# Optimization experiments

Hardware: AMD Instinct MI355X
Metric: run time of the kernel (lower is better)

The kernel has to match this reference:

```python
import jax, jax.numpy as jnp
import numpy as np
import math

DIM = 96; HEADS = 3; WS = 4; SS = 2; RES = 48; B = 2
N = WS ** 3  # tokens per window
LOG2_8 = math.log2(8.0)


def _rel_coords_table():
    c = np.arange(-(WS - 1), WS, dtype=np.float32)
    t = np.stack(np.meshgrid(c, c, c, indexing='ij'), axis=-1)
    t = t / (WS - 1)
    t = t * 8.0
    t = np.sign(t) * np.log2(np.abs(t) + 1.0) / LOG2_8
    return t.reshape(-1, 3)


def _rel_pos_index():
    coords = np.stack(np.meshgrid(np.arange(WS), np.arange(WS), np.arange(WS), indexing='ij'))
    cf = coords.reshape(3, -1)
    rel = (cf[:, :, None] - cf[:, None, :]).transpose(1, 2, 0).copy()
    rel[:, :, 0] += WS - 1; rel[:, :, 1] += WS - 1; rel[:, :, 2] += WS - 1
    rel[:, :, 0] *= (2 * WS - 1) * (2 * WS - 1)
    rel[:, :, 1] *= (2 * WS - 1)
    return rel.sum(-1).reshape(-1)  # (N*N,)


def _attn_mask():
    H = W = D = RES
    img = np.zeros((H, W, D), np.float32)
    cnt = 0
    sl = (slice(0, -WS), slice(-WS, -SS), slice(-SS, None))
    for h in sl:
        for w in sl:
            for d in sl:
                img[h, w, d] = cnt
                cnt += 1
    m = img.reshape(H // WS, WS, W // WS, WS, D // WS, WS)
    m = m.transpose(0, 2, 4, 1, 3, 5).reshape(-1, N)
    am = m[:, None, :] - m[:, :, None]
    return np.where(am != 0, np.float32(-100.0), np.float32(0.0))  # (nW, N, N)


def _win_part(x):
    Bx, H, W, D, C = x.shape
    x = x.reshape(Bx, H // WS, WS, W // WS, WS, D // WS, WS, C)
    x = x.transpose(0, 1, 3, 5, 2, 4, 6, 7)
    return x.reshape(-1, N, C)


def _win_rev(w, Bx, H, W, D):
    C = w.shape[-1]
    x = w.reshape(Bx, H // WS, W // WS, D // WS, WS, WS, WS, C)
    x = x.transpose(0, 1, 4, 2, 5, 3, 6, 7)
    return x.reshape(Bx, H, W, D, C)


def _ln(x, g, b, eps=1e-5):
    mu = jnp.mean(x, axis=-1, keepdims=True)
    var = jnp.mean(jnp.square(x - mu), axis=-1, keepdims=True)
    return (x - mu) * jax.lax.rsqrt(var + eps) * g + b


def setup_inputs() -> dict:
    key = jax.random.key(0)
    ks = jax.random.split(key, 8)
    s = 0.02
    return {
        'x': jax.random.normal(ks[0], (B, RES, RES, RES, DIM), jnp.float32),
        'qkv_w': jax.random.normal(ks[1], (3 * DIM, DIM), jnp.float32) * s,
        'q_bias': jnp.zeros((DIM,), jnp.float32),
        'v_bias': jnp.zeros((DIM,), jnp.float32),
        'logit_scale': jnp.full((HEADS, 1, 1), math.log(10.0), jnp.float32),
        'cpb_w1': jax.random.normal(ks[2], (512, 3), jnp.float32) * s,
        'cpb_b1': jnp.zeros((512,), jnp.float32),
        'cpb_w2': jax.random.normal(ks[3], (HEADS, 512), jnp.float32) * s,
        'proj_w': jax.random.normal(ks[4], (DIM, DIM), jnp.float32) * s,
        'proj_b': jnp.zeros((DIM,), jnp.float32),
        'norm1_g': jnp.ones((DIM,), jnp.float32),
        'norm1_b': jnp.zeros((DIM,), jnp.float32),
        'fc1_w': jax.random.normal(ks[5], (4 * DIM, DIM), jnp.float32) * s,
        'fc1_b': jnp.zeros((4 * DIM,), jnp.float32),
        'fc2_w': jax.random.normal(ks[6], (DIM, 4 * DIM), jnp.float32) * s,
        'fc2_b': jnp.zeros((DIM,), jnp.float32),
        'norm2_g': jnp.ones((DIM,), jnp.float32),
        'norm2_b': jnp.zeros((DIM,), jnp.float32),
    }


def reference(x, qkv_w, q_bias, v_bias, logit_scale, cpb_w1, cpb_b1, cpb_w2,
              proj_w, proj_b, norm1_g, norm1_b, fc1_w, fc1_b, fc2_w, fc2_b,
              norm2_g, norm2_b):
    Bx, H, W, D, C = x.shape
    hd = C // HEADS
    rct = jnp.asarray(_rel_coords_table())
    rpi = _rel_pos_index()
    amask = jnp.asarray(_attn_mask())  # (nW, N, N)

    # cyclic shift + window partition
    shifted = jnp.roll(x, (-SS, -SS, -SS), axis=(1, 2, 3))
    xw = _win_part(shifted)  # (B*nW, N, C)
    B_ = xw.shape[0]; nW = B_ // Bx

    # qkv (k has no bias in SwinV2)
    bias = jnp.concatenate([q_bias, jnp.zeros_like(q_bias), v_bias])
    qkv = (xw @ qkv_w.T + bias).reshape(B_, N, 3, HEADS, hd).transpose(2, 0, 3, 1, 4)
    q, k, v = qkv[0], qkv[1], qkv[2]

    # cosine attention with clamped learnable logit scale
    qn = q / jnp.maximum(jnp.linalg.norm(q, axis=-1, keepdims=True), 1e-12)
    kn = k / jnp.maximum(jnp.linalg.norm(k, axis=-1, keepdims=True), 1e-12)
    attn = jnp.einsum('bhnd,bhmd->bhnm', qn, kn)
    scale = jnp.exp(jnp.minimum(logit_scale, math.log(1.0 / 0.01)))  # (HEADS,1,1)
    attn = attn * scale[None]

    # continuous relative position bias via small MLP + lookup
    tbl = jax.nn.relu(rct @ cpb_w1.T + cpb_b1) @ cpb_w2.T  # (T, HEADS)
    rpb = tbl[rpi].reshape(N, N, HEADS).transpose(2, 0, 1)
    rpb = 16.0 * jax.nn.sigmoid(rpb)
    attn = attn + rpb[None]

    # shift-window mask + softmax
    attn = attn.reshape(Bx, nW, HEADS, N, N) + amask[None, :, None]
    attn = jax.nn.softmax(attn.reshape(B_, HEADS, N, N), axis=-1)

    out = jnp.einsum('bhnm,bhmd->bnhd', attn, v).reshape(B_, N, C)
    out = out @ proj_w.T + proj_b

    # reverse windows + reverse shift
    aw = _win_rev(out.reshape(B_, WS, WS, WS, C), Bx, H, W, D)
    aw = jnp.roll(aw, (SS, SS, SS), axis=(1, 2, 3))

    # SwinV2 post-norm residuals
    x = x + _ln(aw, norm1_g, norm1_b)
    h = jax.nn.gelu(x @ fc1_w.T + fc1_b, approximate=False) @ fc2_w.T + fc2_b
    x = x + _ln(h, norm2_g, norm2_b)
    return x
```

## Files before the change

kernel.cpp:

```cpp
#include <hip/hip_runtime.h>
#include <math.h>

#define RES   48
#define WS    4
#define SSH   2
#define DIM   96
#define HEADS 3
#define HD    32
#define NTOK  64
#define NWAX  12
#define NWIN  (NWAX*NWAX*NWAX)

#define TSTR 104
#define VSTR 72
#define PSTR 72
#define H_STR 392

typedef float f32x4 __attribute__((ext_vector_type(4)));
typedef short s16x8 __attribute__((ext_vector_type(8)));

__device__ __forceinline__ short f2bf(float f) {
    unsigned u = __builtin_bit_cast(unsigned, f);
    u = (u + 0x7FFFu + ((u >> 16) & 1u)) >> 16;
    return (short)u;
}
__device__ __forceinline__ float bf2f(short s) {
    unsigned u = ((unsigned)(unsigned short)s) << 16;
    return __builtin_bit_cast(float, u);
}
__device__ __forceinline__ float gelu_f(float a) {
    float z = a*(1.5957691216057308f + 0.07135481627159927f*a*a);
    return a / (1.0f + __expf(-z));
}
__device__ __forceinline__ int region(int g) {
    return (g < RES - WS) ? 0 : ((g < RES - SSH) ? 1 : 2);
}

__global__ void prep_kernel(const float* __restrict__ cw1, const float* __restrict__ cb1,
                            const float* __restrict__ cw2,
                            const float* __restrict__ fc1_w, const float* __restrict__ fc2_w,
                            const float* __restrict__ qkv_w, const float* __restrict__ proj_w,
                            float* __restrict__ tbl,
                            short* __restrict__ w1p, short* __restrict__ w2p,
                            short* __restrict__ qkvp, short* __restrict__ projp) {
    int bid = blockIdx.x;
    if (bid < 343) {
        __shared__ float hid[512];
        int ti = bid;
        int a = ti / 49, b = (ti / 7) % 7, c = ti % 7;
        float comp[3] = {(float)(a - 3), (float)(b - 3), (float)(c - 3)};
        float f[3];
        #pragma unroll
        for (int k = 0; k < 3; ++k) {
            float u = (comp[k] / 3.0f) * 8.0f;
            float s = (u > 0.f) ? 1.f : ((u < 0.f) ? -1.f : 0.f);
            f[k] = s * log2f(fabsf(u) + 1.0f) * (1.0f / 3.0f);
        }
        for (int j = threadIdx.x; j < 512; j += blockDim.x) {
            float acc = cb1[j] + f[0]*cw1[j*3+0] + f[1]*cw1[j*3+1] + f[2]*cw1[j*3+2];
            hid[j] = fmaxf(acc, 0.f);
        }
        __syncthreads();
        int tid = threadIdx.x;
        if (tid < 192) {
            int h = tid >> 6, lane = tid & 63;
            float p = 0.f;
            for (int j = lane; j < 512; j += 64) p += cw2[h*512 + j] * hid[j];
            #pragma unroll
            for (int off = 32; off; off >>= 1) p += __shfl_down(p, off, 64);
            if (lane == 0) tbl[ti*3 + h] = p;
        }
    } else if (bid < 343 + 144) {
        int i = (bid - 343)*256 + threadIdx.x;
        if (i >= 36864) return;
        {
            int o = i / 96, c = i - o*96;
            int tile = (o >> 4)*3 + (c >> 5);
            int lane = ((c >> 3) & 3)*16 + (o & 15);
            w1p[tile*512 + lane*8 + (c & 7)] = f2bf(fc1_w[i]);
        }
        {
            int co = i / 384, oo = i - co*384;
            int tile = (co >> 4)*12 + (oo >> 5);
            int lane = ((oo >> 3) & 3)*16 + (co & 15);
            w2p[tile*512 + lane*8 + (oo & 7)] = f2bf(fc2_w[i]);
        }
    } else {
        int i = (bid - 487)*256 + threadIdx.x;
        if (i < 288*96) {
            int o = i / 96, c = i - o*96;
            int tile = (o >> 4)*3 + (c >> 5);
            int lane = ((c >> 3) & 3)*16 + (o & 15);
            qkvp[tile*512 + lane*8 + (c & 7)] = f2bf(qkv_w[i]);
        }
        if (i < 96*96) {
            int co = i / 96, k = i - co*96;
            int tile = (co >> 4)*3 + (k >> 5);
            int lane = ((k >> 3) & 3)*16 + (co & 15);
            projp[tile*512 + lane*8 + (k & 7)] = f2bf(proj_w[i]);
        }
    }
}

__global__ void rpb_kernel(const float* __restrict__ tbl, float* __restrict__ rpb) {
    int bi = blockIdx.x;
    int h = bi >> 6, i = bi & 63;
    int j = threadIdx.x;
    int hi = i >> 4, wi = (i >> 2) & 3, di = i & 3;
    int hj = j >> 4, wj = (j >> 2) & 3, dj = j & 3;
    int idx = (hi - hj + 3)*49 + (wi - wj + 3)*7 + (di - dj + 3);
    float v = tbl[idx*3 + h];
    rpb[(h*64 + i)*64 + j] = 16.0f / (1.0f + expf(-v));
}

__global__ __launch_bounds__(256, 2)
void swin_fused_kernel(const float* __restrict__ x, const short* __restrict__ qkvp,
                       const float* __restrict__ q_bias, const float* __restrict__ v_bias,
                       const float* __restrict__ logit_scale,
                       const short* __restrict__ projp, const float* __restrict__ proj_b,
                       const float* __restrict__ rpb,
                       const float* __restrict__ g1, const float* __restrict__ b1v,
                       const short* __restrict__ w1p, const float* __restrict__ fc1_b,
                       const short* __restrict__ w2p, const float* __restrict__ fc2_b,
                       const float* __restrict__ g2, const float* __restrict__ b2v,
                       float* __restrict__ out) {
    __shared__ __align__(16) char pool[64768];
    int*   xbase = (int*)(pool + 0);
    int*   cnt_s = (int*)(pool + 256);
    float* knorm = (float*)(pool + 512);
    short* x_s   = (short*)(pool + 1280);
    short* q_s   = (short*)(pool + 14592);
    short* k_s   = (short*)(pool + 27904);
    short* vT    = (short*)(pool + 41216);
    short* p_s   = (short*)(pool + 55040);
    short* x1b   = x_s;
    short* hb    = (short*)(pool + 14592);
    short* ao_s  = q_s;

    int tid = threadIdx.x;
    int l   = tid & 63;
    int w   = __builtin_amdgcn_readfirstlane(tid >> 6);
    int lc  = l & 15;
    int lg  = l >> 4;

    int wid = blockIdx.x;
    int b   = wid / NWIN;
    int rem = wid - b*NWIN;
    int wh = rem / (NWAX*NWAX);
    int ww = (rem / NWAX) % NWAX;
    int wd = rem % NWAX;

    if (tid < NTOK) {
        int t = tid;
        int lh = t >> 4, lw = (t >> 2) & 3, ld = t & 3;
        int gh = wh*WS + lh, gw = ww*WS + lw, gd = wd*WS + ld;
        int sh = (gh + SSH) % RES, sw = (gw + SSH) % RES, sd = (gd + SSH) % RES;
        xbase[t] = (((b*RES + sh)*RES + sw)*RES + sd)*DIM;
        cnt_s[t] = region(gh)*9 + region(gw)*3 + region(gd);
    }
    __syncthreads();

    for (int idx = tid; idx < NTOK*12; idx += 256) {
        int r = idx / 12, g = idx - r*12;
        const float* src = x + xbase[r] + g*8;
        float4 a = *reinterpret_cast<const float4*>(src);
        float4 c = *reinterpret_cast<const float4*>(src + 4);
        s16x8 v;
        v[0]=f2bf(a.x); v[1]=f2bf(a.y); v[2]=f2bf(a.z); v[3]=f2bf(a.w);
        v[4]=f2bf(c.x); v[5]=f2bf(c.y); v[6]=f2bf(c.z); v[7]=f2bf(c.w);
        *reinterpret_cast<s16x8*>(&x_s[r*TSTR + g*8]) = v;
    }
    __syncthreads();

    {
        s16x8 af[3][4];
        #pragma unroll
        for (int ks = 0; ks < 3; ++ks)
            #pragma unroll
            for (int m = 0; m < 4; ++m)
                af[ks][m] = *reinterpret_cast<const s16x8*>(&x_s[(m*16+lc)*TSTR + ks*32 + lg*8]);

        for (int nt = w; nt < 18; nt += 4) {
            int col = nt*16 + lc;
            float bias = 0.f;
            if (nt < 6) bias = q_bias[col];
            else if (nt >= 12) bias = v_bias[col - 192];
            f32x4 C[4];
            #pragma unroll
            for (int m = 0; m < 4; ++m) C[m] = f32x4{bias, bias, bias, bias};
            #pragma unroll
            for (int ks = 0; ks < 3; ++ks) {
                s16x8 bf = *reinterpret_cast<const s16x8*>(&qkvp[(nt*3+ks)*512 + l*8]);
                #pragma unroll
                for (int m = 0; m < 4; ++m)
                    C[m] = __builtin_amdgcn_mfma_f32_16x16x32_bf16(af[ks][m], bf, C[m], 0, 0, 0);
            }
            if (nt < 6) {
                #pragma unroll
                for (int m = 0; m < 4; ++m)
                    #pragma unroll
                    for (int r = 0; r < 4; ++r)
                        q_s[(m*16+lg*4+r)*TSTR + col] = f2bf(C[m][r]);
            } else if (nt < 12) {
                #pragma unroll
                for (int m = 0; m < 4; ++m)
                    #pragma unroll
                    for (int r = 0; r < 4; ++r)
                        k_s[(m*16+lg*4+r)*TSTR + col - 96] = f2bf(C[m][r]);
            } else {
                #pragma unroll
                for (int m = 0; m < 4; ++m)
                    #pragma unroll
                    for (int r = 0; r < 4; ++r)
                        vT[(col-192)*VSTR + m*16+lg*4+r] = f2bf(C[m][r]);
            }
        }
    }
    __syncthreads();

    if (tid < 192) {
        int h = tid >> 6, i = tid & 63;
        float n = 0.f;
        #pragma unroll
        for (int c = 0; c < 4; ++c) {
            s16x8 v = *reinterpret_cast<const s16x8*>(&k_s[i*TSTR + h*32 + c*8]);
            #pragma unroll
            for (int e = 0; e < 8; ++e) { float f = bf2f(v[e]); n += f*f; }
        }
        knorm[h*64 + i] = 1.0f / fmaxf(sqrtf(n), 1e-12f);

        s16x8 qv[4];
        float qn = 0.f;
        #pragma unroll
        for (int c = 0; c < 4; ++c) {
            qv[c] = *reinterpret_cast<const s16x8*>(&q_s[i*TSTR + h*32 + c*8]);
            #pragma unroll
            for (int e = 0; e < 8; ++e) { float f = bf2f(qv[c][e]); qn += f*f; }
        }
        float sc = __expf(fminf(logit_scale[h], 4.605170185988092f));
        float qr = sc / fmaxf(sqrtf(qn), 1e-12f);
        #pragma unroll
        for (int c = 0; c < 4; ++c) {
            s16x8 o;
            #pragma unroll
            for (int e = 0; e < 8; ++e) o[e] = f2bf(bf2f(qv[c][e]) * qr);
            *reinterpret_cast<s16x8*>(&q_s[i*TSTR + h*32 + c*8]) = o;
        }
    }
    __syncthreads();

    f32x4 sc_[3][4];
    {
        s16x8 aq[3];
        #pragma unroll
        for (int h = 0; h < 3; ++h)
            aq[h] = *reinterpret_cast<const s16x8*>(&q_s[(w*16+lc)*TSTR + h*32 + lg*8]);
        #pragma unroll
        for (int h = 0; h < 3; ++h)
            #pragma unroll
            for (int nt = 0; nt < 4; ++nt) {
                s16x8 bk = *reinterpret_cast<const s16x8*>(&k_s[(nt*16+lc)*TSTR + h*32 + lg*8]);
                sc_[h][nt] = __builtin_amdgcn_mfma_f32_16x16x32_bf16(aq[h], bk, f32x4{0.f,0.f,0.f,0.f}, 0, 0, 0);
            }
    }

    int ci[4];
    #pragma unroll
    for (int r = 0; r < 4; ++r) ci[r] = cnt_s[w*16 + lg*4 + r];
    int cjv[4];
    #pragma unroll
    for (int nt = 0; nt < 4; ++nt) cjv[nt] = cnt_s[nt*16 + lc];

    #pragma unroll
    for (int h = 0; h < 3; ++h) {
        #pragma unroll
        for (int nt = 0; nt < 4; ++nt) {
            float kn = knorm[h*64 + nt*16 + lc];
            int cj = cjv[nt];
            #pragma unroll
            for (int r = 0; r < 4; ++r) {
                int row = w*16 + lg*4 + r;
                float s = sc_[h][nt][r]*kn + rpb[(h*64 + row)*64 + nt*16 + lc];
                if (ci[r] != cj) s -= 100.0f;
                sc_[h][nt][r] = s;
            }
        }
        float linv[4];
        #pragma unroll
        for (int r = 0; r < 4; ++r) {
            float mm = fmaxf(fmaxf(sc_[h][0][r], sc_[h][1][r]), fmaxf(sc_[h][2][r], sc_[h][3][r]));
            #pragma unroll
            for (int msk = 1; msk < 16; msk <<= 1) mm = fmaxf(mm, __shfl_xor(mm, msk, 64));
            float ll = 0.f;
            #pragma unroll
            for (int nt = 0; nt < 4; ++nt) {
                float ee = __expf(sc_[h][nt][r] - mm);
                sc_[h][nt][r] = ee;
                ll += ee;
            }
            #pragma unroll
            for (int msk = 1; msk < 16; msk <<= 1) ll += __shfl_xor(ll, msk, 64);
            linv[r] = 1.0f / ll;
        }
        #pragma unroll
        for (int nt = 0; nt < 4; ++nt)
            #pragma unroll
            for (int r = 0; r < 4; ++r)
                p_s[(w*16+lg*4+r)*PSTR + nt*16 + lc] = f2bf(sc_[h][nt][r]);

        f32x4 o0 = {0.f,0.f,0.f,0.f}, o1 = {0.f,0.f,0.f,0.f};
        #pragma unroll
        for (int ks = 0; ks < 2; ++ks) {
            s16x8 ap = *reinterpret_cast<const s16x8*>(&p_s[(w*16+lc)*PSTR + ks*32 + lg*8]);
            s16x8 b0 = *reinterpret_cast<const s16x8*>(&vT[(h*32 + lc)*VSTR + ks*32 + lg*8]);
            s16x8 b1 = *reinterpret_cast<const s16x8*>(&vT[(h*32 + 16 + lc)*VSTR + ks*32 + lg*8]);
            o0 = __builtin_amdgcn_mfma_f32_16x16x32_bf16(ap, b0, o0, 0, 0, 0);
            o1 = __builtin_amdgcn_mfma_f32_16x16x32_bf16(ap, b1, o1, 0, 0, 0);
        }
        #pragma unroll
        for (int r = 0; r < 4; ++r) {
            ao_s[(w*16+lg*4+r)*TSTR + h*32 + lc]      = f2bf(o0[r]*linv[r]);
            ao_s[(w*16+lg*4+r)*TSTR + h*32 + 16 + lc] = f2bf(o1[r]*linv[r]);
        }
    }

    float yv[6][4];
    {
        s16x8 aa[3];
        #pragma unroll
        for (int ks = 0; ks < 3; ++ks)
            aa[ks] = *reinterpret_cast<const s16x8*>(&ao_s[(w*16+lc)*TSTR + ks*32 + lg*8]);
        #pragma unroll
        for (int nt = 0; nt < 6; ++nt) {
            float bias = proj_b[nt*16 + lc];
            f32x4 C = f32x4{bias, bias, bias, bias};
            #pragma unroll
            for (int ks = 0; ks < 3; ++ks) {
                s16x8 bf = *reinterpret_cast<const s16x8*>(&projp[(nt*3+ks)*512 + l*8]);
                C = __builtin_amdgcn_mfma_f32_16x16x32_bf16(aa[ks], bf, C, 0, 0, 0);
            }
            #pragma unroll
            for (int r = 0; r < 4; ++r) yv[nt][r] = C[r];
        }
    }
    __syncthreads();

    float x1v[6][4];
    #pragma unroll
    for (int r = 0; r < 4; ++r) {
        float s = 0.f, sq = 0.f;
        #pragma unroll
        for (int n = 0; n < 6; ++n) { float v = yv[n][r]; s += v; sq += v*v; }
        #pragma unroll
        for (int m = 1; m < 16; m <<= 1) { s += __shfl_xor(s, m, 64); sq += __shfl_xor(sq, m, 64); }
        float mu  = s * (1.0f/DIM);
        float var = sq * (1.0f/DIM) - mu*mu;
        float rs  = rsqrtf(fmaxf(var, 0.f) + 1e-5f);
        int t = w*16 + lg*4 + r;
        #pragma unroll
        for (int n = 0; n < 6; ++n) {
            int c = n*16 + lc;
            float xf = bf2f(x_s[t*TSTR + c]);
            float v = xf + (yv[n][r] - mu)*rs*g1[c] + b1v[c];
            x1v[n][r] = v;
            x1b[t*TSTR + c] = f2bf(v);
        }
    }
    __syncthreads();

    {
        f32x4 acc1[4][6];
        #pragma unroll
        for (int n = 0; n < 6; ++n) {
            float bb = fc1_b[w*96 + n*16 + lc];
            #pragma unroll
            for (int m = 0; m < 4; ++m) acc1[m][n] = f32x4{bb, bb, bb, bb};
        }
        #pragma unroll
        for (int ks = 0; ks < 3; ++ks) {
            s16x8 af[4];
            #pragma unroll
            for (int m = 0; m < 4; ++m)
                af[m] = *reinterpret_cast<const s16x8*>(&x1b[(m*16 + lc)*TSTR + ks*32 + lg*8]);
            #pragma unroll
            for (int n = 0; n < 6; ++n) {
                s16x8 bf = *reinterpret_cast<const s16x8*>(&w1p[((w*6 + n)*3 + ks)*512 + l*8]);
                #pragma unroll
                for (int m = 0; m < 4; ++m)
                    acc1[m][n] = __builtin_amdgcn_mfma_f32_16x16x32_bf16(af[m], bf, acc1[m][n], 0, 0, 0);
            }
        }
        #pragma unroll
        for (int m = 0; m < 4; ++m) {
            #pragma unroll
            for (int n = 0; n < 6; ++n) {
                int col = w*96 + n*16 + lc;
                #pragma unroll
                for (int r = 0; r < 4; ++r) {
                    int row = m*16 + lg*4 + r;
                    hb[row*H_STR + col] = f2bf(gelu_f(acc1[m][n][r]));
                }
            }
        }
    }
    __syncthreads();

    {
        f32x4 acc2[6];
        #pragma unroll
        for (int n = 0; n < 6; ++n) {
            float bb = fc2_b[n*16 + lc];
            acc2[n] = f32x4{bb, bb, bb, bb};
        }
        #pragma unroll
        for (int ks = 0; ks < 12; ++ks) {
            s16x8 af = *reinterpret_cast<const s16x8*>(&hb[(w*16 + lc)*H_STR + ks*32 + lg*8]);
            #pragma unroll
            for (int n = 0; n < 6; ++n) {
                s16x8 bf = *reinterpret_cast<const s16x8*>(&w2p[(n*12 + ks)*512 + l*8]);
                acc2[n] = __builtin_amdgcn_mfma_f32_16x16x32_bf16(af, bf, acc2[n], 0, 0, 0);
            }
        }
        #pragma unroll
        for (int r = 0; r < 4; ++r) {
            float s = 0.f, sq = 0.f;
            #pragma unroll
            for (int n = 0; n < 6; ++n) { float v = acc2[n][r]; s += v; sq += v*v; }
            #pragma unroll
            for (int m = 1; m < 16; m <<= 1) { s += __shfl_xor(s, m, 64); sq += __shfl_xor(sq, m, 64); }
            float mu  = s * (1.0f/DIM);
            float var = sq * (1.0f/DIM) - mu*mu;
            float rs  = rsqrtf(fmaxf(var, 0.f) + 1e-5f);
            int t = w*16 + lg*4 + r;
            int xb = xbase[t];
            #pragma unroll
            for (int n = 0; n < 6; ++n) {
                int c = n*16 + lc;
                out[xb + c] = x1v[n][r] + (acc2[n][r] - mu)*rs*g2[c] + b2v[c];
            }
        }
    }
}

extern "C" void kernel_launch(void* const* d_in, const int* in_sizes, int n_in,
                              void* d_out, int out_size, void* d_ws, size_t ws_size,
                              hipStream_t stream) {
    const float* x      = (const float*)d_in[0];
    const float* qkv_w  = (const float*)d_in[1];
    const float* q_bias = (const float*)d_in[2];
    const float* v_bias = (const float*)d_in[3];
    const float* lscale = (const float*)d_in[4];
    const float* cpb_w1 = (const float*)d_in[5];
    const float* cpb_b1 = (const float*)d_in[6];
    const float* cpb_w2 = (const float*)d_in[7];
    const float* proj_w = (const float*)d_in[8];
    const float* proj_b = (const float*)d_in[9];
    const float* n1g    = (const float*)d_in[10];
    const float* n1b    = (const float*)d_in[11];
    const float* fc1_w  = (const float*)d_in[12];
    const float* fc1_b  = (const float*)d_in[13];
    const float* fc2_w  = (const float*)d_in[14];
    const float* fc2_b  = (const float*)d_in[15];
    const float* n2g    = (const float*)d_in[16];
    const float* n2b    = (const float*)d_in[17];
    float* out = (float*)d_out;

    char* wsb = (char*)d_ws;
    float* tbl  = (float*)wsb;
    float* rpb  = (float*)(wsb + 8192);
    short* w1p  = (short*)(wsb + 65536);
    short* w2p  = (short*)(wsb + 65536 + 73728);
    short* qkvp = (short*)(wsb + 65536 + 147456);
    short* projp= qkvp + 27648;

    prep_kernel<<<595, 256, 0, stream>>>(cpb_w1, cpb_b1, cpb_w2, fc1_w, fc2_w,
                                         qkv_w, proj_w, tbl, w1p, w2p, qkvp, projp);
    rpb_kernel<<<192, 64, 0, stream>>>(tbl, rpb);
    swin_fused_kernel<<<2*NWIN, 256, 0, stream>>>(x, qkvp, q_bias, v_bias, lscale,
                                                  projp, proj_b, rpb,
                                                  n1g, n1b, w1p, fc1_b, w2p, fc2_b,
                                                  n2g, n2b, out);
}
```

Measured before the change: 194.0 us.

## Split MLP hidden into two halves to shrink LDS and raise occupancy

```diff
diff --git a/kernel.cpp b/kernel.cpp
--- a/kernel.cpp
+++ b/kernel.cpp
@@ -14,7 +14,7 @@
 #define TSTR 104
 #define VSTR 72
 #define PSTR 72
-#define H_STR 392
+#define HSTR 200
 
 typedef float f32x4 __attribute__((ext_vector_type(4)));
 typedef short s16x8 __attribute__((ext_vector_type(8)));
@@ -27,6 +27,11 @@
 __device__ __forceinline__ float bf2f(short s) {
     unsigned u = ((unsigned)(unsigned short)s) << 16;
     return __builtin_bit_cast(float, u);
+}
+__device__ __forceinline__ unsigned cvt_pk(float lo, float hi) {
+    unsigned r;
+    asm("v_cvt_pk_bf16_f32 %0, %1, %2" : "=v"(r) : "v"(lo), "v"(hi));
+    return r;
 }
 __device__ __forceinline__ float gelu_f(float a) {
     float z = a*(1.5957691216057308f + 0.07135481627159927f*a*a);
@@ -75,7 +80,9 @@
         if (i >= 36864) return;
         {
             int o = i / 96, c = i - o*96;
-            int tile = (o >> 4)*3 + (c >> 5);
+            int H = o / 192, rem = o - H*192;
+            int wv = rem / 48, n3 = (rem - wv*48) >> 4;
+            int tile = ((H*12 + wv*3 + n3)*3) + (c >> 5);
             int lane = ((c >> 3) & 3)*16 + (o & 15);
             w1p[tile*512 + lane*8 + (c & 7)] = f2bf(fc1_w[i]);
         }
@@ -113,7 +120,7 @@
     rpb[(h*64 + i)*64 + j] = 16.0f / (1.0f + expf(-v));
 }
 
-__global__ __launch_bounds__(256, 2)
+__global__ __launch_bounds__(256, 3)
 void swin_fused_kernel(const float* __restrict__ x, const short* __restrict__ qkvp,
                        const float* __restrict__ q_bias, const float* __restrict__ v_bias,
                        const float* __restrict__ logit_scale,
@@ -124,18 +131,17 @@
                        const short* __restrict__ w2p, const float* __restrict__ fc2_b,
                        const float* __restrict__ g2, const float* __restrict__ b2v,
                        float* __restrict__ out) {
-    __shared__ __align__(16) char pool[64768];
+    __shared__ __align__(16) char pool[54272];
     int*   xbase = (int*)(pool + 0);
     int*   cnt_s = (int*)(pool + 256);
-    float* knorm = (float*)(pool + 512);
-    short* x_s   = (short*)(pool + 1280);
-    short* q_s   = (short*)(pool + 14592);
-    short* k_s   = (short*)(pool + 27904);
-    short* vT    = (short*)(pool + 41216);
-    short* p_s   = (short*)(pool + 55040);
+    short* x_s   = (short*)(pool + 512);
+    short* q_s   = (short*)(pool + 13824);
+    short* k_s   = (short*)(pool + 27136);
+    short* vT    = (short*)(pool + 40448);
+    short* p_s   = k_s;
+    short* ao_s  = q_s;
     short* x1b   = x_s;
-    short* hb    = (short*)(pool + 14592);
-    short* ao_s  = q_s;
+    short* hb    = (short*)(pool + 13824);
 
     int tid = threadIdx.x;
     int l   = tid & 63;
@@ -160,15 +166,32 @@
     }
     __syncthreads();
 
+    int ci[4], cjv[4];
+    #pragma unroll
+    for (int r = 0; r < 4; ++r) ci[r] = cnt_s[w*16 + lg*4 + r];
+    #pragma unroll
+    for (int nt = 0; nt < 4; ++nt) cjv[nt] = cnt_s[nt*16 + lc];
+    float biasv[3][4][4];
+    #pragma unroll
+    for (int h = 0; h < 3; ++h)
+        #pragma unroll
+        for (int nt = 0; nt < 4; ++nt)
+            #pragma unroll
+            for (int r = 0; r < 4; ++r) {
+                int row = w*16 + lg*4 + r;
+                float bv = rpb[(h*64 + row)*64 + nt*16 + lc];
+                biasv[h][nt][r] = (ci[r] != cjv[nt]) ? bv - 100.0f : bv;
+            }
+
     for (int idx = tid; idx < NTOK*12; idx += 256) {
         int r = idx / 12, g = idx - r*12;
         const float* src = x + xbase[r] + g*8;
         float4 a = *reinterpret_cast<const float4*>(src);
         float4 c = *reinterpret_cast<const float4*>(src + 4);
-        s16x8 v;
-        v[0]=f2bf(a.x); v[1]=f2bf(a.y); v[2]=f2bf(a.z); v[3]=f2bf(a.w);
-        v[4]=f2bf(c.x); v[5]=f2bf(c.y); v[6]=f2bf(c.z); v[7]=f2bf(c.w);
-        *reinterpret_cast<s16x8*>(&x_s[r*TSTR + g*8]) = v;
+        uint4 v;
+        v.x = cvt_pk(a.x, a.y); v.y = cvt_pk(a.z, a.w);
+        v.z = cvt_pk(c.x, c.y); v.w = cvt_pk(c.z, c.w);
+        *reinterpret_cast<uint4*>(&x_s[r*TSTR + g*8]) = v;
     }
     __syncthreads();
 
@@ -197,54 +220,81 @@
             }
             if (nt < 6) {
                 #pragma unroll
-                for (int m = 0; m < 4; ++m)
-                    #pragma unroll
-                    for (int r = 0; r < 4; ++r)
-                        q_s[(m*16+lg*4+r)*TSTR + col] = f2bf(C[m][r]);
+                for (int m = 0; m < 4; ++m) {
+                    unsigned pA = cvt_pk(C[m][0], C[m][1]);
+                    unsigned pB = cvt_pk(C[m][2], C[m][3]);
+                    int row = m*16 + lg*4;
+                    q_s[(row+0)*TSTR + col] = (short)pA;
+                    q_s[(row+1)*TSTR + col] = (short)(pA >> 16);
+                    q_s[(row+2)*TSTR + col] = (short)pB;
+                    q_s[(row+3)*TSTR + col] = (short)(pB >> 16);
+                }
             } else if (nt < 12) {
                 #pragma unroll
-                for (int m = 0; m < 4; ++m)
-                    #pragma unroll
-                    for (int r = 0; r < 4; ++r)
-                        k_s[(m*16+lg*4+r)*TSTR + col - 96] = f2bf(C[m][r]);
+                for (int m = 0; m < 4; ++m) {
+                    unsigned pA = cvt_pk(C[m][0], C[m][1]);
+                    unsigned pB = cvt_pk(C[m][2], C[m][3]);
+                    int row = m*16 + lg*4;
+                    k_s[(row+0)*TSTR + col - 96] = (short)pA;
+                    k_s[(row+1)*TSTR + col - 96] = (short)(pA >> 16);
+                    k_s[(row+2)*TSTR + col - 96] = (short)pB;
+                    k_s[(row+3)*TSTR + col - 96] = (short)(pB >> 16);
+                }
             } else {
                 #pragma unroll
-                for (int m = 0; m < 4; ++m)
-                    #pragma unroll
-                    for (int r = 0; r < 4; ++r)
-                        vT[(col-192)*VSTR + m*16+lg*4+r] = f2bf(C[m][r]);
-            }
-        }
-    }
-    __syncthreads();
-
-    if (tid < 192) {
-        int h = tid >> 6, i = tid & 63;
-        float n = 0.f;
-        #pragma unroll
-        for (int c = 0; c < 4; ++c) {
-            s16x8 v = *reinterpret_cast<const s16x8*>(&k_s[i*TSTR + h*32 + c*8]);
-            #pragma unroll
-            for (int e = 0; e < 8; ++e) { float f = bf2f(v[e]); n += f*f; }
-        }
-        knorm[h*64 + i] = 1.0f / fmaxf(sqrtf(n), 1e-12f);
-
-        s16x8 qv[4];
-        float qn = 0.f;
-        #pragma unroll
-        for (int c = 0; c < 4; ++c) {
-            qv[c] = *reinterpret_cast<const s16x8*>(&q_s[i*TSTR + h*32 + c*8]);
-            #pragma unroll
-            for (int e = 0; e < 8; ++e) { float f = bf2f(qv[c][e]); qn += f*f; }
-        }
-        float sc = __expf(fminf(logit_scale[h], 4.605170185988092f));
-        float qr = sc / fmaxf(sqrtf(qn), 1e-12f);
-        #pragma unroll
-        for (int c = 0; c < 4; ++c) {
-            s16x8 o;
-            #pragma unroll
-            for (int e = 0; e < 8; ++e) o[e] = f2bf(bf2f(qv[c][e]) * qr);
-            *reinterpret_cast<s16x8*>(&q_s[i*TSTR + h*32 + c*8]) = o;
+                for (int m = 0; m < 4; ++m) {
+                    uint2 pv;
+                    pv.x = cvt_pk(C[m][0], C[m][1]);
+                    pv.y = cvt_pk(C[m][2], C[m][3]);
+                    *reinterpret_cast<uint2*>(&vT[(col-192)*VSTR + m*16 + lg*4]) = pv;
+                }
+            }
+        }
+    }
+    __syncthreads();
+
+    if (w < 3) {
+        int h = w, i = l;
+        {
+            s16x8 kv[4];
+            float kn = 0.f;
+            #pragma unroll
+            for (int c = 0; c < 4; ++c) {
+                kv[c] = *reinterpret_cast<const s16x8*>(&k_s[i*TSTR + h*32 + c*8]);
+                #pragma unroll
+                for (int e = 0; e < 8; ++e) { float f = bf2f(kv[c][e]); kn += f*f; }
+            }
+            float kr = 1.0f / fmaxf(sqrtf(kn), 1e-12f);
+            #pragma unroll
+            for (int c = 0; c < 4; ++c) {
+                uint4 o;
+                o.x = cvt_pk(bf2f(kv[c][0])*kr, bf2f(kv[c][1])*kr);
+                o.y = cvt_pk(bf2f(kv[c][2])*kr, bf2f(kv[c][3])*kr);
+                o.z = cvt_pk(bf2f(kv[c][4])*kr, bf2f(kv[c][5])*kr);
+                o.w = cvt_pk(bf2f(kv[c][6])*kr, bf2f(kv[c][7])*kr);
+                *reinterpret_cast<uint4*>(&k_s[i*TSTR + h*32 + c*8]) = o;
+            }
+        }
+        {
+            s16x8 qv[4];
+            float qn = 0.f;
+            #pragma unroll
+            for (int c = 0; c < 4; ++c) {
+                qv[c] = *reinterpret_cast<const s16x8*>(&q_s[i*TSTR + h*32 + c*8]);
+                #pragma unroll
+                for (int e = 0; e < 8; ++e) { float f = bf2f(qv[c][e]); qn += f*f; }
+            }
+            float sc = __expf(fminf(logit_scale[h], 4.605170185988092f));
+            float qr = sc / fmaxf(sqrtf(qn), 1e-12f);
+            #pragma unroll
+            for (int c = 0; c < 4; ++c) {
+                uint4 o;
+                o.x = cvt_pk(bf2f(qv[c][0])*qr, bf2f(qv[c][1])*qr);
+                o.y = cvt_pk(bf2f(qv[c][2])*qr, bf2f(qv[c][3])*qr);
+                o.z = cvt_pk(bf2f(qv[c][4])*qr, bf2f(qv[c][5])*qr);
+                o.w = cvt_pk(bf2f(qv[c][6])*qr, bf2f(qv[c][7])*qr);
+                *reinterpret_cast<uint4*>(&q_s[i*TSTR + h*32 + c*8]) = o;
+            }
         }
     }
     __syncthreads();
@@ -263,28 +313,15 @@
                 sc_[h][nt] = __builtin_amdgcn_mfma_f32_16x16x32_bf16(aq[h], bk, f32x4{0.f,0.f,0.f,0.f}, 0, 0, 0);
             }
     }
-
-    int ci[4];
-    #pragma unroll
-    for (int r = 0; r < 4; ++r) ci[r] = cnt_s[w*16 + lg*4 + r];
-    int cjv[4];
-    #pragma unroll
-    for (int nt = 0; nt < 4; ++nt) cjv[nt] = cnt_s[nt*16 + lc];
+    __syncthreads();
 
     #pragma unroll
     for (int h = 0; h < 3; ++h) {
         #pragma unroll
-        for (int nt = 0; nt < 4; ++nt) {
-            float kn = knorm[h*64 + nt*16 + lc];
-            int cj = cjv[nt];
-            #pragma unroll
-            for (int r = 0; r < 4; ++r) {
-                int row = w*16 + lg*4 + r;
-                float s = sc_[h][nt][r]*kn + rpb[(h*64 + row)*64 + nt*16 + lc];
-                if (ci[r] != cj) s -= 100.0f;
-                sc_[h][nt][r] = s;
-            }
-        }
+        for (int nt = 0; nt < 4; ++nt)
+            #pragma unroll
+            for (int r = 0; r < 4; ++r)
+                sc_[h][nt][r] += biasv[h][nt][r];
         float linv[4];
         #pragma unroll
         for (int r = 0; r < 4; ++r) {
@@ -303,10 +340,15 @@
             linv[r] = 1.0f / ll;
         }
         #pragma unroll
-        for (int nt = 0; nt < 4; ++nt)
-            #pragma unroll
-            for (int r = 0; r < 4; ++r)
-                p_s[(w*16+lg*4+r)*PSTR + nt*16 + lc] = f2bf(sc_[h][nt][r]);
+        for (int nt = 0; nt < 4; ++nt) {
+            unsigned pA = cvt_pk(sc_[h][nt][0], sc_[h][nt][1]);
+            unsigned pB = cvt_pk(sc_[h][nt][2], sc_[h][nt][3]);
+            int row = w*16 + lg*4;
+            p_s[(row+0)*PSTR + nt*16 + lc] = (short)pA;
+            p_s[(row+1)*PSTR + nt*16 + lc] = (short)(pA >> 16);
+            p_s[(row+2)*PSTR + nt*16 + lc] = (short)pB;
+            p_s[(row+3)*PSTR + nt*16 + lc] = (short)(pB >> 16);
+        }
 
         f32x4 o0 = {0.f,0.f,0.f,0.f}, o1 = {0.f,0.f,0.f,0.f};
         #pragma unroll
@@ -317,10 +359,20 @@
             o0 = __builtin_amdgcn_mfma_f32_16x16x32_bf16(ap, b0, o0, 0, 0, 0);
             o1 = __builtin_amdgcn_mfma_f32_16x16x32_bf16(ap, b1, o1, 0, 0, 0);
         }
-        #pragma unroll
-        for (int r = 0; r < 4; ++r) {
-            ao_s[(w*16+lg*4+r)*TSTR + h*32 + lc]      = f2bf(o0[r]*linv[r]);
-            ao_s[(w*16+lg*4+r)*TSTR + h*32 + 16 + lc] = f2bf(o1[r]*linv[r]);
+        {
+            unsigned pA = cvt_pk(o0[0]*linv[0], o0[1]*linv[1]);
+            unsigned pB = cvt_pk(o0[2]*linv[2], o0[3]*linv[3]);
+            unsigned pC = cvt_pk(o1[0]*linv[0], o1[1]*linv[1]);
+            unsigned pD = cvt_pk(o1[2]*linv[2], o1[3]*linv[3]);
+            int row = w*16 + lg*4;
+            ao_s[(row+0)*TSTR + h*32 + lc]      = (short)pA;
+            ao_s[(row+1)*TSTR + h*32 + lc]      = (short)(pA >> 16);
+            ao_s[(row+2)*TSTR + h*32 + lc]      = (short)pB;
+            ao_s[(row+3)*TSTR + h*32 + lc]      = (short)(pB >> 16);
+            ao_s[(row+0)*TSTR + h*32 + 16 + lc] = (short)pC;
+            ao_s[(row+1)*TSTR + h*32 + 16 + lc] = (short)(pC >> 16);
+            ao_s[(row+2)*TSTR + h*32 + 16 + lc] = (short)pD;
+            ao_s[(row+3)*TSTR + h*32 + 16 + lc] = (short)(pD >> 16);
         }
     }
 
@@ -358,86 +410,90 @@
         float rs  = rsqrtf(fmaxf(var, 0.f) + 1e-5f);
         int t = w*16 + lg*4 + r;
         #pragma unroll
+        for (int n2 = 0; n2 < 3; ++n2) {
+            int c0 = n2*32 + lc;
+            float v0 = bf2f(x_s[t*TSTR + c0])      + (yv[n2*2][r]   - mu)*rs*g1[c0]      + b1v[c0];
+            float v1 = bf2f(x_s[t*TSTR + c0 + 16]) + (yv[n2*2+1][r] - mu)*rs*g1[c0+16]   + b1v[c0+16];
+            x1v[n2*2][r] = v0; x1v[n2*2+1][r] = v1;
+            unsigned pk = cvt_pk(v0, v1);
+            x1b[t*TSTR + c0]      = (short)pk;
+            x1b[t*TSTR + c0 + 16] = (short)(pk >> 16);
+        }
+    }
+    __syncthreads();
+
+    f32x4 acc2[6];
+    #pragma unroll
+    for (int n = 0; n < 6; ++n) {
+        float bb = fc2_b[n*16 + lc];
+        acc2[n] = f32x4{bb, bb, bb, bb};
+    }
+    #pragma unroll
+    for (int H = 0; H < 2; ++H) {
+        f32x4 acc1[4][3];
+        #pragma unroll
+        for (int n = 0; n < 3; ++n) {
+            float bb = fc1_b[H*192 + w*48 + n*16 + lc];
+            #pragma unroll
+            for (int m = 0; m < 4; ++m) acc1[m][n] = f32x4{bb, bb, bb, bb};
+        }
+        #pragma unroll
+        for (int ks = 0; ks < 3; ++ks) {
+            s16x8 af[4];
+            #pragma unroll
+            for (int m = 0; m < 4; ++m)
+                af[m] = *reinterpret_cast<const s16x8*>(&x1b[(m*16 + lc)*TSTR + ks*32 + lg*8]);
+            #pragma unroll
+            for (int n = 0; n < 3; ++n) {
+                s16x8 bf = *reinterpret_cast<const s16x8*>(&w1p[((H*12 + w*3 + n)*3 + ks)*512 + l*8]);
+                #pragma unroll
+                for (int m = 0; m < 4; ++m)
+                    acc1[m][n] = __builtin_amdgcn_mfma_f32_16x16x32_bf16(af[m], bf, acc1[m][n], 0, 0, 0);
+            }
+        }
+        #pragma unroll
+        for (int m = 0; m < 4; ++m) {
+            #pragma unroll
+            for (int n = 0; n < 3; ++n) {
+                int col = w*48 + n*16 + lc;
+                unsigned pA = cvt_pk(gelu_f(acc1[m][n][0]), gelu_f(acc1[m][n][1]));
+                unsigned pB = cvt_pk(gelu_f(acc1[m][n][2]), gelu_f(acc1[m][n][3]));
+                int row = m*16 + lg*4;
+                hb[(row+0)*HSTR + col] = (short)pA;
+                hb[(row+1)*HSTR + col] = (short)(pA >> 16);
+                hb[(row+2)*HSTR + col] = (short)pB;
+                hb[(row+3)*HSTR + col] = (short)(pB >> 16);
+            }
+        }
+        __syncthreads();
+        #pragma unroll
+        for (int ksp = 0; ksp < 6; ++ksp) {
+            s16x8 af = *reinterpret_cast<const s16x8*>(&hb[(w*16 + lc)*HSTR + ksp*32 + lg*8]);
+            #pragma unroll
+            for (int n = 0; n < 6; ++n) {
+                s16x8 bf = *reinterpret_cast<const s16x8*>(&w2p[(n*12 + H*6 + ksp)*512 + l*8]);
+                acc2[n] = __builtin_amdgcn_mfma_f32_16x16x32_bf16(af, bf, acc2[n], 0, 0, 0);
+            }
+        }
+        if (H == 0) __syncthreads();
+    }
+
+    #pragma unroll
+    for (int r = 0; r < 4; ++r) {
+        float s = 0.f, sq = 0.f;
+        #pragma unroll
+        for (int n = 0; n < 6; ++n) { float v = acc2[n][r]; s += v; sq += v*v; }
+        #pragma unroll
+        for (int m = 1; m < 16; m <<= 1) { s += __shfl_xor(s, m, 64); sq += __shfl_xor(sq, m, 64); }
+        float mu  = s * (1.0f/DIM);
+        float var = sq * (1.0f/DIM) - mu*mu;
+        float rs  = rsqrtf(fmaxf(var, 0.f) + 1e-5f);
+        int t = w*16 + lg*4 + r;
+        int xb = xbase[t];
+        #pragma unroll
         for (int n = 0; n < 6; ++n) {
             int c = n*16 + lc;
-            float xf = bf2f(x_s[t*TSTR + c]);
-            float v = xf + (yv[n][r] - mu)*rs*g1[c] + b1v[c];
-            x1v[n][r] = v;
-            x1b[t*TSTR + c] = f2bf(v);
-        }
-    }
-    __syncthreads();
-
-    {
-        f32x4 acc1[4][6];
-        #pragma unroll
-        for (int n = 0; n < 6; ++n) {
-            float bb = fc1_b[w*96 + n*16 + lc];
-            #pragma unroll
-            for (int m = 0; m < 4; ++m) acc1[m][n] = f32x4{bb, bb, bb, bb};
-        }
-        #pragma unroll
-        for (int ks = 0; ks < 3; ++ks) {
-            s16x8 af[4];
-            #pragma unroll
-            for (int m = 0; m < 4; ++m)
-                af[m] = *reinterpret_cast<const s16x8*>(&x1b[(m*16 + lc)*TSTR + ks*32 + lg*8]);
-            #pragma unroll
-            for (int n = 0; n < 6; ++n) {
-                s16x8 bf = *reinterpret_cast<const s16x8*>(&w1p[((w*6 + n)*3 + ks)*512 + l*8]);
-                #pragma unroll
-                for (int m = 0; m < 4; ++m)
-                    acc1[m][n] = __builtin_amdgcn_mfma_f32_16x16x32_bf16(af[m], bf, acc1[m][n], 0, 0, 0);
-            }
-        }
-        #pragma unroll
-        for (int m = 0; m < 4; ++m) {
-            #pragma unroll
-            for (int n = 0; n < 6; ++n) {
-                int col = w*96 + n*16 + lc;
-                #pragma unroll
-                for (int r = 0; r < 4; ++r) {
-                    int row = m*16 + lg*4 + r;
-                    hb[row*H_STR + col] = f2bf(gelu_f(acc1[m][n][r]));
-                }
-            }
-        }
-    }
-    __syncthreads();
-
-    {
-        f32x4 acc2[6];
-        #pragma unroll
-        for (int n = 0; n < 6; ++n) {
-            float bb = fc2_b[n*16 + lc];
-            acc2[n] = f32x4{bb, bb, bb, bb};
-        }
-        #pragma unroll
-        for (int ks = 0; ks < 12; ++ks) {
-            s16x8 af = *reinterpret_cast<const s16x8*>(&hb[(w*16 + lc)*H_STR + ks*32 + lg*8]);
-            #pragma unroll
-            for (int n = 0; n < 6; ++n) {
-                s16x8 bf = *reinterpret_cast<const s16x8*>(&w2p[(n*12 + ks)*512 + l*8]);
-                acc2[n] = __builtin_amdgcn_mfma_f32_16x16x32_bf16(af, bf, acc2[n], 0, 0, 0);
-            }
-        }
-        #pragma unroll
-        for (int r = 0; r < 4; ++r) {
-            float s = 0.f, sq = 0.f;
-            #pragma unroll
-            for (int n = 0; n < 6; ++n) { float v = acc2[n][r]; s += v; sq += v*v; }
-            #pragma unroll
-            for (int m = 1; m < 16; m <<= 1) { s += __shfl_xor(s, m, 64); sq += __shfl_xor(sq, m, 64); }
-            float mu  = s * (1.0f/DIM);
-            float var = sq * (1.0f/DIM) - mu*mu;
-            float rs  = rsqrtf(fmaxf(var, 0.f) + 1e-5f);
-            int t = w*16 + lg*4 + r;
-            int xb = xbase[t];
-            #pragma unroll
-            for (int n = 0; n < 6; ++n) {
-                int c = n*16 + lc;
-                out[xb + c] = x1v[n][r] + (acc2[n][r] - mu)*rs*g2[c] + b2v[c];
-            }
+            out[xb + c] = x1v[n][r] + (acc2[n][r] - mu)*rs*g2[c] + b2v[c];
         }
     }
 }
```

Result: slower. 300.9 us (+55.1%).
